# Performance work log

Measured on AMD Instinct MI355X. Metric: run time of the kernel, lower is better.

Reference implementation:

```python
import jax, jax.numpy as jnp
import numpy as np

S, IN, OUT = 2048, 512, 512
H, KV = 16, 4            # query heads, kv heads (cross-broadcast + averaged)
DQ = DK = DV = 64        # per-head embedding dims


def setup_inputs() -> dict:
    key = jax.random.key(0)
    ks = jax.random.split(key, 5)
    lim_in = 1.0 / np.sqrt(IN)
    lim_o = 1.0 / np.sqrt(H * DV)
    x = jax.random.normal(ks[0], (S, IN), dtype=jnp.float32)
    Wq = jax.random.uniform(ks[1], (H * DQ, IN), jnp.float32, -lim_in, lim_in)
    Wk = jax.random.uniform(ks[2], (KV * DK, IN), jnp.float32, -lim_in, lim_in)
    Wv = jax.random.uniform(ks[3], (KV * DV, IN), jnp.float32, -lim_in, lim_in)
    Wo = jax.random.uniform(ks[4], (OUT, H * DV), jnp.float32, -lim_o, lim_o)
    return {"x": x, "Wq": Wq, "Wk": Wk, "Wv": Wv, "Wo": Wo}


def reference(x, Wq, Wk, Wv, Wo):
    seq = x.shape[0]
    # projections (eqx.nn.Linear: y = W @ x, no bias)
    q = (x @ Wq.T).reshape(seq, H, DQ)    # [S, H, DQ]
    k = (x @ Wk.T).reshape(seq, KV, DK)   # [S, KV, DK]
    v = (x @ Wv.T).reshape(seq, KV, DV)   # [S, KV, DV]
    # cross-broadcast every kv head against every query head -> [KV, H, S, S]
    scores = jnp.einsum('shd,tkd->khst', q, k) / jnp.sqrt(jnp.asarray(DK, x.dtype))
    # NOTE: original applies causal mask whenever `mask is not None`; the
    # boolean flag is always passed, so masking is effectively always on.
    causal = jnp.tril(jnp.ones((seq, seq), dtype=bool))
    scores = jnp.where(causal, scores, -jnp.inf)
    w = jax.nn.softmax(scores, axis=-1)   # [KV, H, S, S]
    # attn @ V, then sum over kv heads and average by KV
    o = jnp.einsum('khst,tkd->shd', w, v) / KV  # [S, H, DV]
    return o.reshape(seq, H * DV) @ Wo.T        # [S, OUT]
```

## Files before the change

### kernel.cpp

```cpp
#include <hip/hip_runtime.h>
#include <hip/hip_bf16.h>

#define SEQ   2048
#define INF_  512
#define HQ    16
#define KVH   4
#define DH    64
#define NQ    (HQ*DH)
#define NKV   (KVH*DH)
#define OUTD  512

typedef short v8s __attribute__((ext_vector_type(8)));
typedef float v4f __attribute__((ext_vector_type(4)));

static __device__ __forceinline__ float bf2f(unsigned short u) {
    union { unsigned int i; float f; } c;
    c.i = ((unsigned int)u) << 16;
    return c.f;
}
static __device__ __forceinline__ unsigned short f2bf(float f) {
    union { float f; unsigned int i; } c; c.f = f;
    unsigned int lsb = (c.i >> 16) & 1u;
    c.i += 0x7fffu + lsb;
    return (unsigned short)(c.i >> 16);
}
static __device__ __forceinline__ unsigned int f2bf2(float lo, float hi) {
    union { __hip_bfloat162 h; unsigned int u; } c;
    c.h = __float22bfloat162_rn(make_float2(lo, hi));
    return c.u;
}
static __device__ __forceinline__ v8s pack8(v4f a, v4f b) {
    union { v8s s; uint4 u; } c;
    c.u = make_uint4(f2bf2(a[0], a[1]), f2bf2(a[2], a[3]),
                     f2bf2(b[0], b[1]), f2bf2(b[2], b[3]));
    return c.s;
}

static __device__ __forceinline__ void gll16(const void* g, void* l) {
    __builtin_amdgcn_global_load_lds(
        (const __attribute__((address_space(1))) void*)g,
        (__attribute__((address_space(3))) void*)l, 16, 0, 0);
}

static __device__ __forceinline__ void stage_tile(
    const unsigned short* __restrict__ src, int stride, int kb,
    unsigned short* ldsbase, int w, int lane)
{
#pragma unroll
    for (int i = 0; i < 2; i++) {
        const int rl = w * 16 + i * 8 + (lane >> 3);
        const int kc = ((lane & 7) ^ (rl & 7)) * 8;
        gll16(src + (size_t)rl * stride + kb + kc,
              ldsbase + (w * 16 + i * 8) * 64);
    }
}

static __device__ __forceinline__ void stage_tile32(
    const unsigned short* __restrict__ src, int stride, int kb,
    unsigned short* ldsbase, int w, int lane)
{
    const int rl = w * 8 + (lane >> 3);
    const int kc = ((lane & 7) ^ (rl & 7)) * 8;
    gll16(src + (size_t)rl * stride + kb + kc,
          ldsbase + (w * 8) * 64);
}

#define QSCALE 0.180336880f

__global__ __launch_bounds__(256) void cast_all(
    const float* __restrict__ x,  const float* __restrict__ Wq,
    const float* __restrict__ Wk, const float* __restrict__ Wv,
    const float* __restrict__ Wo,
    unsigned short* __restrict__ xb,  unsigned short* __restrict__ Wqb,
    unsigned short* __restrict__ Wkb, unsigned short* __restrict__ Wvb,
    unsigned short* __restrict__ Wob)
{
    size_t i = ((size_t)blockIdx.x * 256 + threadIdx.x) * 8;
    const float* s; unsigned short* d; size_t off;
    if (i < 1048576)      { s = x;  d = xb;  off = i; }
    else if (i < 1572864) { s = Wq; d = Wqb; off = i - 1048576; }
    else if (i < 1703936) { s = Wk; d = Wkb; off = i - 1572864; }
    else if (i < 1835008) { s = Wv; d = Wvb; off = i - 1703936; }
    else                  { s = Wo; d = Wob; off = i - 1835008; }
    float4 a = *(const float4*)(s + off);
    float4 b = *(const float4*)(s + off + 4);
    *(uint4*)(d + off) = make_uint4(f2bf2(a.x, a.y), f2bf2(a.z, a.w),
                                    f2bf2(b.x, b.y), f2bf2(b.z, b.w));
}

__global__ __launch_bounds__(256, 4) void gemm_qkv(
    const unsigned short* __restrict__ xb,
    const unsigned short* __restrict__ Wqb,
    const unsigned short* __restrict__ Wkb,
    const unsigned short* __restrict__ Wvb,
    unsigned short* __restrict__ Qg,
    unsigned short* __restrict__ Kg,
    unsigned short* __restrict__ Vg)
{
    __shared__ unsigned short Asb[2][4096];
    __shared__ unsigned short Bsb[2][4096];

    const int m0 = blockIdx.x * 64;
    const int n0 = blockIdx.y * 64;

    const unsigned short* Bp; int role;
    if (n0 < NQ)            { Bp = Wqb + (size_t)n0 * INF_;              role = 0; }
    else if (n0 < NQ + NKV) { Bp = Wkb + (size_t)(n0 - NQ) * INF_;       role = 1; }
    else                    { Bp = Wvb + (size_t)(n0 - NQ - NKV) * INF_; role = 2; }

    const int tid = threadIdx.x;
    const int w = tid >> 6, lane = tid & 63;
    const int n = lane & 15, quad = lane >> 4;
    const int m7 = n & 7;
    const int r0w = (w & 1) * 32, c0w = (w >> 1) * 32;
    const unsigned short* Ap = xb + (size_t)m0 * INF_;

    v4f acc[2][2];
#pragma unroll
    for (int rt = 0; rt < 2; rt++)
#pragma unroll
        for (int ct = 0; ct < 2; ct++) acc[rt][ct] = (v4f){0.f,0.f,0.f,0.f};

    stage_tile(Ap, INF_, 0, &Asb[0][0], w, lane);
    stage_tile(Bp, INF_, 0, &Bsb[0][0], w, lane);

    for (int kb = 0; kb < INF_; kb += 64) {
        const int buf = (kb >> 6) & 1;
        __syncthreads();
        if (kb + 64 < INF_) {
            stage_tile(Ap, INF_, kb + 64, &Asb[buf ^ 1][0], w, lane);
            stage_tile(Bp, INF_, kb + 64, &Bsb[buf ^ 1][0], w, lane);
        }
#pragma unroll
        for (int kk = 0; kk < 2; kk++) {
            const int gs = ((kk * 4 + quad) ^ m7) * 8;
            v8s a0 = *(const v8s*)&Asb[buf][(r0w + n) * 64 + gs];
            v8s a1 = *(const v8s*)&Asb[buf][(r0w + 16 + n) * 64 + gs];
            v8s b0 = *(const v8s*)&Bsb[buf][(c0w + n) * 64 + gs];
            v8s b1 = *(const v8s*)&Bsb[buf][(c0w + 16 + n) * 64 + gs];
            acc[0][0] = __builtin_amdgcn_mfma_f32_16x16x32_bf16(a0, b0, acc[0][0], 0, 0, 0);
            acc[0][1] = __builtin_amdgcn_mfma_f32_16x16x32_bf16(a0, b1, acc[0][1], 0, 0, 0);
            acc[1][0] = __builtin_amdgcn_mfma_f32_16x16x32_bf16(a1, b0, acc[1][0], 0, 0, 0);
            acc[1][1] = __builtin_amdgcn_mfma_f32_16x16x32_bf16(a1, b1, acc[1][1], 0, 0, 0);
        }
    }

    const int t = m0 >> 6;
    if (role == 0) {
        unsigned short* base = Qg + ((size_t)(t * 16 + (n0 >> 6))) * 4096;
#pragma unroll
        for (int rt = 0; rt < 2; rt++)
#pragma unroll
            for (int ct = 0; ct < 2; ct++)
#pragma unroll
                for (int reg = 0; reg < 4; reg++) {
                    const int r = r0w + rt * 16 + quad * 4 + reg;
                    const int d = c0w + ct * 16 + n;
                    base[r * 64 + (((d >> 3) ^ (r & 7)) * 8) + (d & 7)] =
                        f2bf(acc[rt][ct][reg] * QSCALE);
                }
    } else if (role == 1) {
        const int g = (n0 - NQ) >> 6;
        unsigned short* base = Kg + ((size_t)(g * 32 + t)) * 4096;
#pragma unroll
        for (int rt = 0; rt < 2; rt++)
#pragma unroll
            for (int ct = 0; ct < 2; ct++)
#pragma unroll
                for (int reg = 0; reg < 4; reg++) {
                    const int r = r0w + rt * 16 + quad * 4 + reg;
                    const int d = c0w + ct * 16 + n;
                    base[r * 64 + (((d >> 3) ^ (r & 7)) * 8) + (d & 7)] =
                        f2bf(acc[rt][ct][reg]);
                }
    } else {
        const int g = (n0 - NQ - NKV) >> 6;
        unsigned short* base = Vg + ((size_t)(g * 32 + t)) * 4096;
#pragma unroll
        for (int rt = 0; rt < 2; rt++)
#pragma unroll
            for (int ct = 0; ct < 2; ct++) {
                const int jb_ = r0w + rt * 16 + quad * 4;
                const int d = c0w + ct * 16 + n;
                const int p = (jb_ & 32) + (((jb_ >> 2) & 3) * 8) + (((jb_ >> 4) & 1) * 4);
                *(uint2*)&base[d * 64 + (((p >> 3) ^ (d & 7)) * 8) + (p & 7)] =
                    make_uint2(f2bf2(acc[rt][ct][0], acc[rt][ct][1]),
                               f2bf2(acc[rt][ct][2], acc[rt][ct][3]));
            }
    }
}

__global__ __launch_bounds__(256, 4) void attn_mfma(
    const unsigned short* __restrict__ Qg,
    const unsigned short* __restrict__ Kg,
    const unsigned short* __restrict__ Vg,
    unsigned short* __restrict__ Oh)
{
    __shared__ unsigned short Ksb[2][4096];
    __shared__ unsigned short Vsb[2][4096];

    const int bx = blockIdx.x;
    const int h  = bx & 15;
    const int p  = (bx >> 4) & 7;
    const int sp = (bx >> 7) & 1;
    const int g  = bx >> 8;
    const int tid = threadIdx.x;
    const int w = tid >> 6, lane = tid & 63;
    const int n = lane & 15, quad = lane >> 4;
    const int m7 = n & 7;

    v8s ones;
#pragma unroll
    for (int i = 0; i < 8; i++) ones[i] = (short)0x3F80;
    const v4f z = (v4f){0.f,0.f,0.f,0.f};

    unsigned short* Ohp = Oh + (size_t)g * ((size_t)SEQ * NQ);

    for (int half = 0; half < 2; half++) {
        const int qi2 = half ? (15 - p) : p;
        const int qbase = qi2 * 128 + sp * 64;
        const int ext = 2 * qi2 + sp + 1;
        const int rowbase = qbase + w * 16;

        if (half) __syncthreads();

        {
            const size_t off = ((size_t)(g * 32)) * 4096 + w * 1024 + lane * 8;
            gll16(Kg + off,       &Ksb[0][w * 1024]);
            gll16(Kg + off + 512, &Ksb[0][w * 1024 + 512]);
            gll16(Vg + off,       &Vsb[0][w * 1024]);
            gll16(Vg + off + 512, &Vsb[0][w * 1024 + 512]);
        }

        v8s qf0, qf1;
        {
            const unsigned short* rp =
                Qg + ((size_t)((2 * qi2 + sp) * 16 + h)) * 4096 + (w * 16 + n) * 64;
            qf0 = *(const v8s*)(rp + (quad ^ m7) * 8);
            qf1 = *(const v8s*)(rp + ((quad + 4) ^ m7) * 8);
        }

        v4f Lacc = (v4f){0.f,0.f,0.f,0.f};
        v4f Oacc[4];
#pragma unroll
        for (int dt = 0; dt < 4; dt++) Oacc[dt] = (v4f){0.f,0.f,0.f,0.f};

        for (int tt = 0; tt < ext; tt++) {
            const int buf = tt & 1;
            __syncthreads();
            if (tt + 1 < ext) {
                const size_t off = ((size_t)(g * 32 + tt + 1)) * 4096 + w * 1024 + lane * 8;
                const int nb = buf ^ 1;
                gll16(Kg + off,       &Ksb[nb][w * 1024]);
                gll16(Kg + off + 512, &Ksb[nb][w * 1024 + 512]);
                gll16(Vg + off,       &Vsb[nb][w * 1024]);
                gll16(Vg + off + 512, &Vsb[nb][w * 1024 + 512]);
            }
            const int t0 = tt * 64;
            const unsigned short* Kb = Ksb[buf];
            const unsigned short* Vb = Vsb[buf];

            v4f sc[4];
            __builtin_amdgcn_s_setprio(1);
#pragma unroll
            for (int jt = 0; jt < 4; jt++) {
                const int kr = (jt * 16 + n) * 64;
                v8s kf0 = *(const v8s*)&Kb[kr + (quad ^ m7) * 8];
                v8s kf1 = *(const v8s*)&Kb[kr + ((quad + 4) ^ m7) * 8];
                v4f tq = __builtin_amdgcn_mfma_f32_16x16x32_bf16(kf0, qf0, z, 0, 0, 0);
                sc[jt] = __builtin_amdgcn_mfma_f32_16x16x32_bf16(kf1, qf1, tq, 0, 0, 0);
            }
            __builtin_amdgcn_s_setprio(0);

            if (t0 + 63 > rowbase) {
                const int qg = rowbase + n;
#pragma unroll
                for (int jt = 0; jt < 4; jt++) {
                    const int jg = t0 + jt * 16 + quad * 4;
#pragma unroll
                    for (int reg = 0; reg < 4; reg++)
                        sc[jt][reg] = (jg + reg <= qg) ? sc[jt][reg] : -INFINITY;
                }
            }
#pragma unroll
            for (int jt = 0; jt < 4; jt++)
#pragma unroll
                for (int reg = 0; reg < 4; reg++)
                    sc[jt][reg] = __builtin_amdgcn_exp2f(sc[jt][reg]);

            v8s pf0 = pack8(sc[0], sc[1]);
            v8s pf1 = pack8(sc[2], sc[3]);

            __builtin_amdgcn_s_setprio(1);
            Lacc = __builtin_amdgcn_mfma_f32_16x16x32_bf16(ones, pf0, Lacc, 0, 0, 0);
            Lacc = __builtin_amdgcn_mfma_f32_16x16x32_bf16(ones, pf1, Lacc, 0, 0, 0);

#pragma unroll
            for (int dt = 0; dt < 4; dt++) {
                const int vr = (dt * 16 + n) * 64;
                v8s vf0 = *(const v8s*)&Vb[vr + (quad ^ m7) * 8];
                v8s vf1 = *(const v8s*)&Vb[vr + ((quad + 4) ^ m7) * 8];
                Oacc[dt] = __builtin_amdgcn_mfma_f32_16x16x32_bf16(vf0, pf0, Oacc[dt], 0, 0, 0);
                Oacc[dt] = __builtin_amdgcn_mfma_f32_16x16x32_bf16(vf1, pf1, Oacc[dt], 0, 0, 0);
            }
            __builtin_amdgcn_s_setprio(0);
        }

        {
            const float inv = 0.25f / Lacc[0];
            const int row = rowbase + n;
            unsigned short* dst = Ohp + (size_t)row * NQ + h * DH + quad * 4;
#pragma unroll
            for (int dt = 0; dt < 4; dt++) {
                uint2 pk = make_uint2(f2bf2(Oacc[dt][0] * inv, Oacc[dt][1] * inv),
                                      f2bf2(Oacc[dt][2] * inv, Oacc[dt][3] * inv));
                *(uint2*)(dst + dt * 16) = pk;
            }
        }
    }
}

__global__ __launch_bounds__(256) void sum4(
    const unsigned short* __restrict__ Oh,
    unsigned short* __restrict__ Os)
{
    const size_t i = ((size_t)blockIdx.x * 256 + threadIdx.x) * 8;
    const size_t plane = (size_t)SEQ * NQ;
    uint4 u0 = *(const uint4*)(Oh + i);
    uint4 u1 = *(const uint4*)(Oh + plane + i);
    uint4 u2 = *(const uint4*)(Oh + 2 * plane + i);
    uint4 u3 = *(const uint4*)(Oh + 3 * plane + i);
    unsigned int ow[4];
#pragma unroll
    for (int q = 0; q < 4; q++) {
        const unsigned int a = ((const unsigned int*)&u0)[q];
        const unsigned int b = ((const unsigned int*)&u1)[q];
        const unsigned int c = ((const unsigned int*)&u2)[q];
        const unsigned int d = ((const unsigned int*)&u3)[q];
        float lo = bf2f((unsigned short)(a & 0xffffu)) + bf2f((unsigned short)(b & 0xffffu))
                 + bf2f((unsigned short)(c & 0xffffu)) + bf2f((unsigned short)(d & 0xffffu));
        float hi = bf2f((unsigned short)(a >> 16)) + bf2f((unsigned short)(b >> 16))
                 + bf2f((unsigned short)(c >> 16)) + bf2f((unsigned short)(d >> 16));
        ow[q] = f2bf2(lo, hi);
    }
    *(uint4*)(Os + i) = make_uint4(ow[0], ow[1], ow[2], ow[3]);
}

__global__ __launch_bounds__(256, 4) void gemm_out(
    const unsigned short* __restrict__ Os,
    const unsigned short* __restrict__ Wob,
    float* __restrict__ C)
{
    __shared__ unsigned short Asb[2][2048];
    __shared__ unsigned short Bsb[2][4096];

    const int m0 = blockIdx.x * 32;
    const int n0 = blockIdx.y * 64;
    const int tid = threadIdx.x;
    const int w = tid >> 6, lane = tid & 63;
    const int n = lane & 15, quad = lane >> 4;
    const int m7 = n & 7;
    const int rw = (w & 1) * 16, cw = (w >> 1) * 32;

    const unsigned short* Ap = Os + (size_t)m0 * NQ;
    const unsigned short* Bp = Wob + (size_t)n0 * NQ;

    v4f acc[2];
    acc[0] = (v4f){0.f,0.f,0.f,0.f};
    acc[1] = (v4f){0.f,0.f,0.f,0.f};

    stage_tile32(Ap, NQ, 0, &Asb[0][0], w, lane);
    stage_tile  (Bp, NQ, 0, &Bsb[0][0], w, lane);

    for (int kb = 0; kb < NQ; kb += 64) {
        const int buf = (kb >> 6) & 1;
        __syncthreads();
        if (kb + 64 < NQ) {
            stage_tile32(Ap, NQ, kb + 64, &Asb[buf ^ 1][0], w, lane);
            stage_tile  (Bp, NQ, kb + 64, &Bsb[buf ^ 1][0], w, lane);
        }
#pragma unroll
        for (int kk = 0; kk < 2; kk++) {
            const int gs = ((kk * 4 + quad) ^ m7) * 8;
            v8s a  = *(const v8s*)&Asb[buf][(rw + n) * 64 + gs];
            v8s b0 = *(const v8s*)&Bsb[buf][(cw + n) * 64 + gs];
            v8s b1 = *(const v8s*)&Bsb[buf][(cw + 16 + n) * 64 + gs];
            acc[0] = __builtin_amdgcn_mfma_f32_16x16x32_bf16(a, b0, acc[0], 0, 0, 0);
            acc[1] = __builtin_amdgcn_mfma_f32_16x16x32_bf16(a, b1, acc[1], 0, 0, 0);
        }
    }

#pragma unroll
    for (int ct = 0; ct < 2; ct++)
#pragma unroll
        for (int reg = 0; reg < 4; reg++) {
            const int row = m0 + rw + quad * 4 + reg;
            const int col = n0 + cw + ct * 16 + n;
            C[(size_t)row * OUTD + col] = acc[ct][reg];
        }
}

extern "C" void kernel_launch(void* const* d_in, const int* in_sizes, int n_in,
                              void* d_out, int out_size, void* d_ws, size_t ws_size,
                              hipStream_t stream) {
    const float* x  = (const float*)d_in[0];
    const float* Wq = (const float*)d_in[1];
    const float* Wk = (const float*)d_in[2];
    const float* Wv = (const float*)d_in[3];
    const float* Wo = (const float*)d_in[4];
    float* out = (float*)d_out;

    char* base = (char*)d_ws;
    unsigned short* Oh  = (unsigned short*)(base);
    unsigned short* xb  = (unsigned short*)(base);
    unsigned short* Wqb = (unsigned short*)(base + 2097152);
    unsigned short* Wkb = (unsigned short*)(base + 3145728);
    unsigned short* Wvb = (unsigned short*)(base + 3407872);
    unsigned short* Qg  = (unsigned short*)(base + 16777216);
    unsigned short* Kg  = (unsigned short*)(base + 20971520);
    unsigned short* Vg  = (unsigned short*)(base + 22020096);
    unsigned short* Wob = (unsigned short*)(base + 23068672);
    unsigned short* Os  = Qg;

    dim3 blk(256);
    cast_all<<<dim3(1152), blk, 0, stream>>>(x, Wq, Wk, Wv, Wo,
                                             xb, Wqb, Wkb, Wvb, Wob);
    gemm_qkv<<<dim3(SEQ / 64, (NQ + 2 * NKV) / 64), blk, 0, stream>>>(
        xb, Wqb, Wkb, Wvb, Qg, Kg, Vg);
    attn_mfma<<<dim3(1024), blk, 0, stream>>>(Qg, Kg, Vg, Oh);
    sum4<<<dim3(1024), blk, 0, stream>>>(Oh, Os);
    gemm_out<<<dim3(SEQ / 32, OUTD / 64), blk, 0, stream>>>(Os, Wob, out);
}
```

Baseline: 142.7 us.

## Software-pipeline QK^T scores one tile ahead of softmax and PV

Restructures the attention inner loop so the QK^T MFMAs for tile t are issued in the same iteration as the mask/exp2/PV work for tile t-1. V gets a third LDS buffer so its tile stays live one extra iteration, and the global base pointers are hoisted. The aim is to overlap the exp/pack latency with matrix work. In exchange it adds LDS (one more 8 KB buffer), more live registers, and an extra loop iteration, which may lower occupancy under launch_bounds(256,4). It also leaves a dead modulo computation in the prefetch index.

```diff
diff --git a/kernel.cpp b/kernel.cpp
--- a/kernel.cpp
+++ b/kernel.cpp
@@ -197,7 +197,7 @@
     unsigned short* __restrict__ Oh)
 {
     __shared__ unsigned short Ksb[2][4096];
-    __shared__ unsigned short Vsb[2][4096];
+    __shared__ unsigned short Vsb[3][4096];
 
     const int bx = blockIdx.x;
     const int h  = bx & 15;
@@ -215,6 +215,8 @@
     const v4f z = (v4f){0.f,0.f,0.f,0.f};
 
     unsigned short* Ohp = Oh + (size_t)g * ((size_t)SEQ * NQ);
+    const unsigned short* Kgp = Kg + ((size_t)(g * 32)) * 4096 + w * 1024 + lane * 8;
+    const unsigned short* Vgp = Vg + ((size_t)(g * 32)) * 4096 + w * 1024 + lane * 8;
 
     for (int half = 0; half < 2; half++) {
         const int qi2 = half ? (15 - p) : p;
@@ -224,13 +226,10 @@
 
         if (half) __syncthreads();
 
-        {
-            const size_t off = ((size_t)(g * 32)) * 4096 + w * 1024 + lane * 8;
-            gll16(Kg + off,       &Ksb[0][w * 1024]);
-            gll16(Kg + off + 512, &Ksb[0][w * 1024 + 512]);
-            gll16(Vg + off,       &Vsb[0][w * 1024]);
-            gll16(Vg + off + 512, &Vsb[0][w * 1024 + 512]);
-        }
+        gll16(Kgp,       &Ksb[0][w * 1024]);
+        gll16(Kgp + 512, &Ksb[0][w * 1024 + 512]);
+        gll16(Vgp,       &Vsb[0][w * 1024]);
+        gll16(Vgp + 512, &Vsb[0][w * 1024 + 512]);
 
         v8s qf0, qf1;
         {
@@ -245,65 +244,99 @@
 #pragma unroll
         for (int dt = 0; dt < 4; dt++) Oacc[dt] = (v4f){0.f,0.f,0.f,0.f};
 
-        for (int tt = 0; tt < ext; tt++) {
-            const int buf = tt & 1;
+        v4f scP0, scP1, scP2, scP3;
+        scP0 = scP1 = scP2 = scP3 = z;
+
+        for (int t = 0; t <= ext; t++) {
+            const int kbuf = t & 1;
             __syncthreads();
-            if (tt + 1 < ext) {
-                const size_t off = ((size_t)(g * 32 + tt + 1)) * 4096 + w * 1024 + lane * 8;
-                const int nb = buf ^ 1;
-                gll16(Kg + off,       &Ksb[nb][w * 1024]);
-                gll16(Kg + off + 512, &Ksb[nb][w * 1024 + 512]);
-                gll16(Vg + off,       &Vsb[nb][w * 1024]);
-                gll16(Vg + off + 512, &Vsb[nb][w * 1024 + 512]);
+            if (t + 1 < ext) {
+                const int kb2 = (t + 1) & 1;
+                int vb2 = t + 1; vb2 -= (vb2 >= 3) ? 3 : 0; vb2 -= (vb2 >= 3) ? 3 : 0;
+                vb2 = (t + 1) % 3;
+                const size_t doff = (size_t)(t + 1) * 4096;
+                gll16(Kgp + doff,       &Ksb[kb2][w * 1024]);
+                gll16(Kgp + doff + 512, &Ksb[kb2][w * 1024 + 512]);
+                gll16(Vgp + doff,       &Vsb[vb2][w * 1024]);
+                gll16(Vgp + doff + 512, &Vsb[vb2][w * 1024 + 512]);
             }
-            const int t0 = tt * 64;
-            const unsigned short* Kb = Ksb[buf];
-            const unsigned short* Vb = Vsb[buf];
-
-            v4f sc[4];
-            __builtin_amdgcn_s_setprio(1);
-#pragma unroll
-            for (int jt = 0; jt < 4; jt++) {
-                const int kr = (jt * 16 + n) * 64;
-                v8s kf0 = *(const v8s*)&Kb[kr + (quad ^ m7) * 8];
-                v8s kf1 = *(const v8s*)&Kb[kr + ((quad + 4) ^ m7) * 8];
-                v4f tq = __builtin_amdgcn_mfma_f32_16x16x32_bf16(kf0, qf0, z, 0, 0, 0);
-                sc[jt] = __builtin_amdgcn_mfma_f32_16x16x32_bf16(kf1, qf1, tq, 0, 0, 0);
+
+            v4f scN0 = z, scN1 = z, scN2 = z, scN3 = z;
+            if (t < ext) {
+                const unsigned short* Kb = Ksb[kbuf];
+                __builtin_amdgcn_s_setprio(1);
+                {
+                    const int kr0 = n * 64;
+                    v8s ka = *(const v8s*)&Kb[kr0 + (quad ^ m7) * 8];
+                    v8s kb_ = *(const v8s*)&Kb[kr0 + ((quad + 4) ^ m7) * 8];
+                    v4f tq = __builtin_amdgcn_mfma_f32_16x16x32_bf16(ka, qf0, z, 0, 0, 0);
+                    scN0 = __builtin_amdgcn_mfma_f32_16x16x32_bf16(kb_, qf1, tq, 0, 0, 0);
+                }
+                {
+                    const int kr1 = (16 + n) * 64;
+                    v8s ka = *(const v8s*)&Kb[kr1 + (quad ^ m7) * 8];
+                    v8s kb_ = *(const v8s*)&Kb[kr1 + ((quad + 4) ^ m7) * 8];
+                    v4f tq = __builtin_amdgcn_mfma_f32_16x16x32_bf16(ka, qf0, z, 0, 0, 0);
+                    scN1 = __builtin_amdgcn_mfma_f32_16x16x32_bf16(kb_, qf1, tq, 0, 0, 0);
+                }
+                {
+                    const int kr2 = (32 + n) * 64;
+                    v8s ka = *(const v8s*)&Kb[kr2 + (quad ^ m7) * 8];
+                    v8s kb_ = *(const v8s*)&Kb[kr2 + ((quad + 4) ^ m7) * 8];
+                    v4f tq = __builtin_amdgcn_mfma_f32_16x16x32_bf16(ka, qf0, z, 0, 0, 0);
+                    scN2 = __builtin_amdgcn_mfma_f32_16x16x32_bf16(kb_, qf1, tq, 0, 0, 0);
+                }
+                {
+                    const int kr3 = (48 + n) * 64;
+                    v8s ka = *(const v8s*)&Kb[kr3 + (quad ^ m7) * 8];
+                    v8s kb_ = *(const v8s*)&Kb[kr3 + ((quad + 4) ^ m7) * 8];
+                    v4f tq = __builtin_amdgcn_mfma_f32_16x16x32_bf16(ka, qf0, z, 0, 0, 0);
+                    scN3 = __builtin_amdgcn_mfma_f32_16x16x32_bf16(kb_, qf1, tq, 0, 0, 0);
+                }
+                __builtin_amdgcn_s_setprio(0);
             }
-            __builtin_amdgcn_s_setprio(0);
-
-            if (t0 + 63 > rowbase) {
-                const int qg = rowbase + n;
-#pragma unroll
-                for (int jt = 0; jt < 4; jt++) {
-                    const int jg = t0 + jt * 16 + quad * 4;
-#pragma unroll
-                    for (int reg = 0; reg < 4; reg++)
-                        sc[jt][reg] = (jg + reg <= qg) ? sc[jt][reg] : -INFINITY;
-                }
+
+            if (t > 0) {
+                const int tp = t - 1;
+                const int t0 = tp * 64;
+                v4f s0 = scP0, s1 = scP1, s2 = scP2, s3 = scP3;
+                if (t0 + 63 > rowbase) {
+                    const int qg = rowbase + n;
+#pragma unroll
+                    for (int reg = 0; reg < 4; reg++) {
+                        s0[reg] = (t0 +  0 + quad * 4 + reg <= qg) ? s0[reg] : -INFINITY;
+                        s1[reg] = (t0 + 16 + quad * 4 + reg <= qg) ? s1[reg] : -INFINITY;
+                        s2[reg] = (t0 + 32 + quad * 4 + reg <= qg) ? s2[reg] : -INFINITY;
+                        s3[reg] = (t0 + 48 + quad * 4 + reg <= qg) ? s3[reg] : -INFINITY;
+                    }
+                }
+#pragma unroll
+                for (int reg = 0; reg < 4; reg++) {
+                    s0[reg] = __builtin_amdgcn_exp2f(s0[reg]);
+                    s1[reg] = __builtin_amdgcn_exp2f(s1[reg]);
+                    s2[reg] = __builtin_amdgcn_exp2f(s2[reg]);
+                    s3[reg] = __builtin_amdgcn_exp2f(s3[reg]);
+                }
+                v8s pf0 = pack8(s0, s1);
+                v8s pf1 = pack8(s2, s3);
+
+                __builtin_amdgcn_s_setprio(1);
+                Lacc = __builtin_amdgcn_mfma_f32_16x16x32_bf16(ones, pf0, Lacc, 0, 0, 0);
+                Lacc = __builtin_amdgcn_mfma_f32_16x16x32_bf16(ones, pf1, Lacc, 0, 0, 0);
+
+                const unsigned short* Vb = Vsb[tp % 3];
+#pragma unroll
+                for (int dt = 0; dt < 4; dt++) {
+                    const int vr = (dt * 16 + n) * 64;
+                    v8s vf0 = *(const v8s*)&Vb[vr + (quad ^ m7) * 8];
+                    v8s vf1 = *(const v8s*)&Vb[vr + ((quad + 4) ^ m7) * 8];
+                    Oacc[dt] = __builtin_amdgcn_mfma_f32_16x16x32_bf16(vf0, pf0, Oacc[dt], 0, 0, 0);
+                    Oacc[dt] = __builtin_amdgcn_mfma_f32_16x16x32_bf16(vf1, pf1, Oacc[dt], 0, 0, 0);
+                }
+                __builtin_amdgcn_s_setprio(0);
             }
-#pragma unroll
-            for (int jt = 0; jt < 4; jt++)
-#pragma unroll
-                for (int reg = 0; reg < 4; reg++)
-                    sc[jt][reg] = __builtin_amdgcn_exp2f(sc[jt][reg]);
-
-            v8s pf0 = pack8(sc[0], sc[1]);
-            v8s pf1 = pack8(sc[2], sc[3]);
-
-            __builtin_amdgcn_s_setprio(1);
-            Lacc = __builtin_amdgcn_mfma_f32_16x16x32_bf16(ones, pf0, Lacc, 0, 0, 0);
-            Lacc = __builtin_amdgcn_mfma_f32_16x16x32_bf16(ones, pf1, Lacc, 0, 0, 0);
-
-#pragma unroll
-            for (int dt = 0; dt < 4; dt++) {
-                const int vr = (dt * 16 + n) * 64;
-                v8s vf0 = *(const v8s*)&Vb[vr + (quad ^ m7) * 8];
-                v8s vf1 = *(const v8s*)&Vb[vr + ((quad + 4) ^ m7) * 8];
-                Oacc[dt] = __builtin_amdgcn_mfma_f32_16x16x32_bf16(vf0, pf0, Oacc[dt], 0, 0, 0);
-                Oacc[dt] = __builtin_amdgcn_mfma_f32_16x16x32_bf16(vf1, pf1, Oacc[dt], 0, 0, 0);
-            }
-            __builtin_amdgcn_s_setprio(0);
+
+            scP0 = scN0; scP1 = scN1; scP2 = scN2; scP3 = scN3;
         }
 
         {
```

Result: no change. 145.1 us (+1.7%).

## Load K/V fragments directly from global memory instead of LDS staging

Applied to the files above, without the earlier changes.

Removes the double-buffered shared-memory staging of K and V tiles and their per-tile barriers. Each wave now reads its K and V MFMA fragments straight from global memory (relying on L1/L2 caching), with the loop body manually unrolled. This eliminates LDS traffic and __syncthreads, but each of the four waves now issues redundant global loads for the same tile, and load latency is no longer hidden by a prefetch.

```diff
diff --git a/kernel.cpp b/kernel.cpp
--- a/kernel.cpp
+++ b/kernel.cpp
@@ -196,9 +196,6 @@
     const unsigned short* __restrict__ Vg,
     unsigned short* __restrict__ Oh)
 {
-    __shared__ unsigned short Ksb[2][4096];
-    __shared__ unsigned short Vsb[2][4096];
-
     const int bx = blockIdx.x;
     const int h  = bx & 15;
     const int p  = (bx >> 4) & 7;
@@ -208,6 +205,8 @@
     const int w = tid >> 6, lane = tid & 63;
     const int n = lane & 15, quad = lane >> 4;
     const int m7 = n & 7;
+    const int fo0 = (quad ^ m7) * 8;
+    const int fo1 = ((quad + 4) ^ m7) * 8;
 
     v8s ones;
 #pragma unroll
@@ -215,29 +214,20 @@
     const v4f z = (v4f){0.f,0.f,0.f,0.f};
 
     unsigned short* Ohp = Oh + (size_t)g * ((size_t)SEQ * NQ);
+    const unsigned short* Kg0 = Kg + (size_t)(g * 32) * 4096;
+    const unsigned short* Vg0 = Vg + (size_t)(g * 32) * 4096;
 
     for (int half = 0; half < 2; half++) {
         const int qi2 = half ? (15 - p) : p;
-        const int qbase = qi2 * 128 + sp * 64;
         const int ext = 2 * qi2 + sp + 1;
-        const int rowbase = qbase + w * 16;
-
-        if (half) __syncthreads();
-
-        {
-            const size_t off = ((size_t)(g * 32)) * 4096 + w * 1024 + lane * 8;
-            gll16(Kg + off,       &Ksb[0][w * 1024]);
-            gll16(Kg + off + 512, &Ksb[0][w * 1024 + 512]);
-            gll16(Vg + off,       &Vsb[0][w * 1024]);
-            gll16(Vg + off + 512, &Vsb[0][w * 1024 + 512]);
-        }
+        const int rowbase = qi2 * 128 + sp * 64 + w * 16;
 
         v8s qf0, qf1;
         {
             const unsigned short* rp =
                 Qg + ((size_t)((2 * qi2 + sp) * 16 + h)) * 4096 + (w * 16 + n) * 64;
-            qf0 = *(const v8s*)(rp + (quad ^ m7) * 8);
-            qf1 = *(const v8s*)(rp + ((quad + 4) ^ m7) * 8);
+            qf0 = *(const v8s*)(rp + fo0);
+            qf1 = *(const v8s*)(rp + fo1);
         }
 
         v4f Lacc = (v4f){0.f,0.f,0.f,0.f};
@@ -245,64 +235,82 @@
 #pragma unroll
         for (int dt = 0; dt < 4; dt++) Oacc[dt] = (v4f){0.f,0.f,0.f,0.f};
 
-        for (int tt = 0; tt < ext; tt++) {
-            const int buf = tt & 1;
-            __syncthreads();
-            if (tt + 1 < ext) {
-                const size_t off = ((size_t)(g * 32 + tt + 1)) * 4096 + w * 1024 + lane * 8;
-                const int nb = buf ^ 1;
-                gll16(Kg + off,       &Ksb[nb][w * 1024]);
-                gll16(Kg + off + 512, &Ksb[nb][w * 1024 + 512]);
-                gll16(Vg + off,       &Vsb[nb][w * 1024]);
-                gll16(Vg + off + 512, &Vsb[nb][w * 1024 + 512]);
-            }
-            const int t0 = tt * 64;
-            const unsigned short* Kb = Ksb[buf];
-            const unsigned short* Vb = Vsb[buf];
-
-            v4f sc[4];
+        for (int t = 0; t < ext; t++) {
+            const unsigned short* Kt = Kg0 + (size_t)t * 4096;
+            const unsigned short* Vt = Vg0 + (size_t)t * 4096;
+
+            v8s kf00 = *(const v8s*)&Kt[( 0 + n) * 64 + fo0];
+            v8s kf01 = *(const v8s*)&Kt[( 0 + n) * 64 + fo1];
+            v8s kf10 = *(const v8s*)&Kt[(16 + n) * 64 + fo0];
+            v8s kf11 = *(const v8s*)&Kt[(16 + n) * 64 + fo1];
+            v8s kf20 = *(const v8s*)&Kt[(32 + n) * 64 + fo0];
+            v8s kf21 = *(const v8s*)&Kt[(32 + n) * 64 + fo1];
+            v8s kf30 = *(const v8s*)&Kt[(48 + n) * 64 + fo0];
+            v8s kf31 = *(const v8s*)&Kt[(48 + n) * 64 + fo1];
+
+            v4f sc0, sc1, sc2, sc3;
             __builtin_amdgcn_s_setprio(1);
-#pragma unroll
-            for (int jt = 0; jt < 4; jt++) {
-                const int kr = (jt * 16 + n) * 64;
-                v8s kf0 = *(const v8s*)&Kb[kr + (quad ^ m7) * 8];
-                v8s kf1 = *(const v8s*)&Kb[kr + ((quad + 4) ^ m7) * 8];
-                v4f tq = __builtin_amdgcn_mfma_f32_16x16x32_bf16(kf0, qf0, z, 0, 0, 0);
-                sc[jt] = __builtin_amdgcn_mfma_f32_16x16x32_bf16(kf1, qf1, tq, 0, 0, 0);
+            {
+                v4f tq = __builtin_amdgcn_mfma_f32_16x16x32_bf16(kf00, qf0, z, 0, 0, 0);
+                sc0 = __builtin_amdgcn_mfma_f32_16x16x32_bf16(kf01, qf1, tq, 0, 0, 0);
+            }
+            {
+                v4f tq = __builtin_amdgcn_mfma_f32_16x16x32_bf16(kf10, qf0, z, 0, 0, 0);
+                sc1 = __builtin_amdgcn_mfma_f32_16x16x32_bf16(kf11, qf1, tq, 0, 0, 0);
+            }
+            {
+                v4f tq = __builtin_amdgcn_mfma_f32_16x16x32_bf16(kf20, qf0, z, 0, 0, 0);
+                sc2 = __builtin_amdgcn_mfma_f32_16x16x32_bf16(kf21, qf1, tq, 0, 0, 0);
+            }
+            {
+                v4f tq = __builtin_amdgcn_mfma_f32_16x16x32_bf16(kf30, qf0, z, 0, 0, 0);
+                sc3 = __builtin_amdgcn_mfma_f32_16x16x32_bf16(kf31, qf1, tq, 0, 0, 0);
             }
             __builtin_amdgcn_s_setprio(0);
 
+            v8s vf00 = *(const v8s*)&Vt[( 0 + n) * 64 + fo0];
+            v8s vf01 = *(const v8s*)&Vt[( 0 + n) * 64 + fo1];
+            v8s vf10 = *(const v8s*)&Vt[(16 + n) * 64 + fo0];
+            v8s vf11 = *(const v8s*)&Vt[(16 + n) * 64 + fo1];
+            v8s vf20 = *(const v8s*)&Vt[(32 + n) * 64 + fo0];
+            v8s vf21 = *(const v8s*)&Vt[(32 + n) * 64 + fo1];
+            v8s vf30 = *(const v8s*)&Vt[(48 + n) * 64 + fo0];
+            v8s vf31 = *(const v8s*)&Vt[(48 + n) * 64 + fo1];
+
+            const int t0 = t * 64;
             if (t0 + 63 > rowbase) {
                 const int qg = rowbase + n;
 #pragma unroll
-                for (int jt = 0; jt < 4; jt++) {
-                    const int jg = t0 + jt * 16 + quad * 4;
-#pragma unroll
-                    for (int reg = 0; reg < 4; reg++)
-                        sc[jt][reg] = (jg + reg <= qg) ? sc[jt][reg] : -INFINITY;
+                for (int reg = 0; reg < 4; reg++) {
+                    sc0[reg] = (t0 +  0 + quad * 4 + reg <= qg) ? sc0[reg] : -INFINITY;
+                    sc1[reg] = (t0 + 16 + quad * 4 + reg <= qg) ? sc1[reg] : -INFINITY;
+                    sc2[reg] = (t0 + 32 + quad * 4 + reg <= qg) ? sc2[reg] : -INFINITY;
+                    sc3[reg] = (t0 + 48 + quad * 4 + reg <= qg) ? sc3[reg] : -INFINITY;
                 }
             }
 #pragma unroll
-            for (int jt = 0; jt < 4; jt++)
-#pragma unroll
-                for (int reg = 0; reg < 4; reg++)
-                    sc[jt][reg] = __builtin_amdgcn_exp2f(sc[jt][reg]);
-
-            v8s pf0 = pack8(sc[0], sc[1]);
-            v8s pf1 = pack8(sc[2], sc[3]);
+            for (int reg = 0; reg < 4; reg++) {
+                sc0[reg] = __builtin_amdgcn_exp2f(sc0[reg]);
+                sc1[reg] = __builtin_amdgcn_exp2f(sc1[reg]);
+                sc2[reg] = __builtin_amdgcn_exp2f(sc2[reg]);
+                sc3[reg] = __builtin_amdgcn_exp2f(sc3[reg]);
+            }
+
+            v8s pf0 = pack8(sc0, sc1);
+            v8s pf1 = pack8(sc2, sc3);
 
             __builtin_amdgcn_s_setprio(1);
             Lacc = __builtin_amdgcn_mfma_f32_16x16x32_bf16(ones, pf0, Lacc, 0, 0, 0);
             Lacc = __builtin_amdgcn_mfma_f32_16x16x32_bf16(ones, pf1, Lacc, 0, 0, 0);
 
-#pragma unroll
-            for (int dt = 0; dt < 4; dt++) {
-                const int vr = (dt * 16 + n) * 64;
-                v8s vf0 = *(const v8s*)&Vb[vr + (quad ^ m7) * 8];
-                v8s vf1 = *(const v8s*)&Vb[vr + ((quad + 4) ^ m7) * 8];
-                Oacc[dt] = __builtin_amdgcn_mfma_f32_16x16x32_bf16(vf0, pf0, Oacc[dt], 0, 0, 0);
-                Oacc[dt] = __builtin_amdgcn_mfma_f32_16x16x32_bf16(vf1, pf1, Oacc[dt], 0, 0, 0);
-            }
+            Oacc[0] = __builtin_amdgcn_mfma_f32_16x16x32_bf16(vf00, pf0, Oacc[0], 0, 0, 0);
+            Oacc[0] = __builtin_amdgcn_mfma_f32_16x16x32_bf16(vf01, pf1, Oacc[0], 0, 0, 0);
+            Oacc[1] = __builtin_amdgcn_mfma_f32_16x16x32_bf16(vf10, pf0, Oacc[1], 0, 0, 0);
+            Oacc[1] = __builtin_amdgcn_mfma_f32_16x16x32_bf16(vf11, pf1, Oacc[1], 0, 0, 0);
+            Oacc[2] = __builtin_amdgcn_mfma_f32_16x16x32_bf16(vf20, pf0, Oacc[2], 0, 0, 0);
+            Oacc[2] = __builtin_amdgcn_mfma_f32_16x16x32_bf16(vf21, pf1, Oacc[2], 0, 0, 0);
+            Oacc[3] = __builtin_amdgcn_mfma_f32_16x16x32_bf16(vf30, pf0, Oacc[3], 0, 0, 0);
+            Oacc[3] = __builtin_amdgcn_mfma_f32_16x16x32_bf16(vf31, pf1, Oacc[3], 0, 0, 0);
             __builtin_amdgcn_s_setprio(0);
         }
 
```

After: 194.7 us. 1.36x slower.

## Process two query heads per attention block to reuse K/V tiles

Applied to the files above, without the earlier changes.

Each attention block now handles a pair of query heads against the same KV head, so every K/V tile staged in shared memory and every K/V fragment read from LDS feeds twice as many MFMAs. The grid is halved and the launch bound relaxed to two blocks per SM to make room for the doubled accumulators and Q fragments. This aims to cut global and LDS traffic per unit of compute, at the cost of fewer blocks, higher register pressure and lower occupancy.

```diff
diff --git a/kernel.cpp b/kernel.cpp
--- a/kernel.cpp
+++ b/kernel.cpp
@@ -190,7 +190,7 @@
     }
 }
 
-__global__ __launch_bounds__(256, 4) void attn_mfma(
+__global__ __launch_bounds__(256, 2) void attn_mfma(
     const unsigned short* __restrict__ Qg,
     const unsigned short* __restrict__ Kg,
     const unsigned short* __restrict__ Vg,
@@ -200,14 +200,16 @@
     __shared__ unsigned short Vsb[2][4096];
 
     const int bx = blockIdx.x;
-    const int h  = bx & 15;
-    const int p  = (bx >> 4) & 7;
-    const int sp = (bx >> 7) & 1;
-    const int g  = bx >> 8;
+    const int hg = bx & 7;
+    const int p  = (bx >> 3) & 7;
+    const int sp = (bx >> 6) & 1;
+    const int g  = bx >> 7;
     const int tid = threadIdx.x;
     const int w = tid >> 6, lane = tid & 63;
     const int n = lane & 15, quad = lane >> 4;
     const int m7 = n & 7;
+    const int fo0 = (quad ^ m7) * 8;
+    const int fo1 = ((quad + 4) ^ m7) * 8;
 
     v8s ones;
 #pragma unroll
@@ -218,9 +220,8 @@
 
     for (int half = 0; half < 2; half++) {
         const int qi2 = half ? (15 - p) : p;
-        const int qbase = qi2 * 128 + sp * 64;
         const int ext = 2 * qi2 + sp + 1;
-        const int rowbase = qbase + w * 16;
+        const int rowbase = qi2 * 128 + sp * 64 + w * 16;
 
         if (half) __syncthreads();
 
@@ -232,18 +233,22 @@
             gll16(Vg + off + 512, &Vsb[0][w * 1024 + 512]);
         }
 
-        v8s qf0, qf1;
+        v8s qa0, qa1, qb0, qb1;
         {
-            const unsigned short* rp =
-                Qg + ((size_t)((2 * qi2 + sp) * 16 + h)) * 4096 + (w * 16 + n) * 64;
-            qf0 = *(const v8s*)(rp + (quad ^ m7) * 8);
-            qf1 = *(const v8s*)(rp + ((quad + 4) ^ m7) * 8);
-        }
-
-        v4f Lacc = (v4f){0.f,0.f,0.f,0.f};
-        v4f Oacc[4];
-#pragma unroll
-        for (int dt = 0; dt < 4; dt++) Oacc[dt] = (v4f){0.f,0.f,0.f,0.f};
+            const unsigned short* rpA =
+                Qg + ((size_t)((2 * qi2 + sp) * 16 + hg * 2)) * 4096 + (w * 16 + n) * 64;
+            const unsigned short* rpB = rpA + 4096;
+            qa0 = *(const v8s*)(rpA + fo0);
+            qa1 = *(const v8s*)(rpA + fo1);
+            qb0 = *(const v8s*)(rpB + fo0);
+            qb1 = *(const v8s*)(rpB + fo1);
+        }
+
+        v4f LA = (v4f){0.f,0.f,0.f,0.f};
+        v4f LB = (v4f){0.f,0.f,0.f,0.f};
+        v4f OA[4], OB[4];
+#pragma unroll
+        for (int dt = 0; dt < 4; dt++) { OA[dt] = z; OB[dt] = z; }
 
         for (int tt = 0; tt < ext; tt++) {
             const int buf = tt & 1;
@@ -256,65 +261,83 @@
                 gll16(Vg + off,       &Vsb[nb][w * 1024]);
                 gll16(Vg + off + 512, &Vsb[nb][w * 1024 + 512]);
             }
-            const int t0 = tt * 64;
             const unsigned short* Kb = Ksb[buf];
             const unsigned short* Vb = Vsb[buf];
 
-            v4f sc[4];
+            v4f sa[4], sb[4];
             __builtin_amdgcn_s_setprio(1);
 #pragma unroll
             for (int jt = 0; jt < 4; jt++) {
                 const int kr = (jt * 16 + n) * 64;
-                v8s kf0 = *(const v8s*)&Kb[kr + (quad ^ m7) * 8];
-                v8s kf1 = *(const v8s*)&Kb[kr + ((quad + 4) ^ m7) * 8];
-                v4f tq = __builtin_amdgcn_mfma_f32_16x16x32_bf16(kf0, qf0, z, 0, 0, 0);
-                sc[jt] = __builtin_amdgcn_mfma_f32_16x16x32_bf16(kf1, qf1, tq, 0, 0, 0);
+                v8s k0 = *(const v8s*)&Kb[kr + fo0];
+                v8s k1 = *(const v8s*)&Kb[kr + fo1];
+                v4f ta = __builtin_amdgcn_mfma_f32_16x16x32_bf16(k0, qa0, z, 0, 0, 0);
+                sa[jt] = __builtin_amdgcn_mfma_f32_16x16x32_bf16(k1, qa1, ta, 0, 0, 0);
+                v4f tb = __builtin_amdgcn_mfma_f32_16x16x32_bf16(k0, qb0, z, 0, 0, 0);
+                sb[jt] = __builtin_amdgcn_mfma_f32_16x16x32_bf16(k1, qb1, tb, 0, 0, 0);
             }
             __builtin_amdgcn_s_setprio(0);
 
+            const int t0 = tt * 64;
             if (t0 + 63 > rowbase) {
                 const int qg = rowbase + n;
 #pragma unroll
                 for (int jt = 0; jt < 4; jt++) {
                     const int jg = t0 + jt * 16 + quad * 4;
 #pragma unroll
-                    for (int reg = 0; reg < 4; reg++)
-                        sc[jt][reg] = (jg + reg <= qg) ? sc[jt][reg] : -INFINITY;
+                    for (int reg = 0; reg < 4; reg++) {
+                        const bool keep = (jg + reg <= qg);
+                        sa[jt][reg] = keep ? sa[jt][reg] : -INFINITY;
+                        sb[jt][reg] = keep ? sb[jt][reg] : -INFINITY;
+                    }
                 }
             }
 #pragma unroll
             for (int jt = 0; jt < 4; jt++)
 #pragma unroll
-                for (int reg = 0; reg < 4; reg++)
-                    sc[jt][reg] = __builtin_amdgcn_exp2f(sc[jt][reg]);
-
-            v8s pf0 = pack8(sc[0], sc[1]);
-            v8s pf1 = pack8(sc[2], sc[3]);
+                for (int reg = 0; reg < 4; reg++) {
+                    sa[jt][reg] = __builtin_amdgcn_exp2f(sa[jt][reg]);
+                    sb[jt][reg] = __builtin_amdgcn_exp2f(sb[jt][reg]);
+                }
+
+            v8s pA0 = pack8(sa[0], sa[1]);
+            v8s pA1 = pack8(sa[2], sa[3]);
+            v8s pB0 = pack8(sb[0], sb[1]);
+            v8s pB1 = pack8(sb[2], sb[3]);
 
             __builtin_amdgcn_s_setprio(1);
-            Lacc = __builtin_amdgcn_mfma_f32_16x16x32_bf16(ones, pf0, Lacc, 0, 0, 0);
-            Lacc = __builtin_amdgcn_mfma_f32_16x16x32_bf16(ones, pf1, Lacc, 0, 0, 0);
+            LA = __builtin_amdgcn_mfma_f32_16x16x32_bf16(ones, pA0, LA, 0, 0, 0);
+            LA = __builtin_amdgcn_mfma_f32_16x16x32_bf16(ones, pA1, LA, 0, 0, 0);
+            LB = __builtin_amdgcn_mfma_f32_16x16x32_bf16(ones, pB0, LB, 0, 0, 0);
+            LB = __builtin_amdgcn_mfma_f32_16x16x32_bf16(ones, pB1, LB, 0, 0, 0);
 
 #pragma unroll
             for (int dt = 0; dt < 4; dt++) {
                 const int vr = (dt * 16 + n) * 64;
-                v8s vf0 = *(const v8s*)&Vb[vr + (quad ^ m7) * 8];
-                v8s vf1 = *(const v8s*)&Vb[vr + ((quad + 4) ^ m7) * 8];
-                Oacc[dt] = __builtin_amdgcn_mfma_f32_16x16x32_bf16(vf0, pf0, Oacc[dt], 0, 0, 0);
-                Oacc[dt] = __builtin_amdgcn_mfma_f32_16x16x32_bf16(vf1, pf1, Oacc[dt], 0, 0, 0);
+                v8s v0 = *(const v8s*)&Vb[vr + fo0];
+                v8s v1 = *(const v8s*)&Vb[vr + fo1];
+                OA[dt] = __builtin_amdgcn_mfma_f32_16x16x32_bf16(v0, pA0, OA[dt], 0, 0, 0);
+                OA[dt] = __builtin_amdgcn_mfma_f32_16x16x32_bf16(v1, pA1, OA[dt], 0, 0, 0);
+                OB[dt] = __builtin_amdgcn_mfma_f32_16x16x32_bf16(v0, pB0, OB[dt], 0, 0, 0);
+                OB[dt] = __builtin_amdgcn_mfma_f32_16x16x32_bf16(v1, pB1, OB[dt], 0, 0, 0);
             }
             __builtin_amdgcn_s_setprio(0);
         }
 
         {
-            const float inv = 0.25f / Lacc[0];
+            const float invA = 0.25f / LA[0];
+            const float invB = 0.25f / LB[0];
             const int row = rowbase + n;
-            unsigned short* dst = Ohp + (size_t)row * NQ + h * DH + quad * 4;
+            unsigned short* dA = Ohp + (size_t)row * NQ + (hg * 2) * DH + quad * 4;
+            unsigned short* dB = dA + DH;
 #pragma unroll
             for (int dt = 0; dt < 4; dt++) {
-                uint2 pk = make_uint2(f2bf2(Oacc[dt][0] * inv, Oacc[dt][1] * inv),
-                                      f2bf2(Oacc[dt][2] * inv, Oacc[dt][3] * inv));
-                *(uint2*)(dst + dt * 16) = pk;
+                uint2 pkA = make_uint2(f2bf2(OA[dt][0] * invA, OA[dt][1] * invA),
+                                       f2bf2(OA[dt][2] * invA, OA[dt][3] * invA));
+                *(uint2*)(dA + dt * 16) = pkA;
+                uint2 pkB = make_uint2(f2bf2(OB[dt][0] * invB, OB[dt][1] * invB),
+                                       f2bf2(OB[dt][2] * invB, OB[dt][3] * invB));
+                *(uint2*)(dB + dt * 16) = pkB;
             }
         }
     }
@@ -427,7 +450,7 @@
                                              xb, Wqb, Wkb, Wvb, Wob);
     gemm_qkv<<<dim3(SEQ / 64, (NQ + 2 * NKV) / 64), blk, 0, stream>>>(
         xb, Wqb, Wkb, Wvb, Qg, Kg, Vg);
-    attn_mfma<<<dim3(1024), blk, 0, stream>>>(Qg, Kg, Vg, Oh);
+    attn_mfma<<<dim3(512), blk, 0, stream>>>(Qg, Kg, Vg, Oh);
     sum4<<<dim3(1024), blk, 0, stream>>>(Oh, Os);
     gemm_out<<<dim3(SEQ / 32, OUTD / 64), blk, 0, stream>>>(Os, Wob, out);
 }
```

Measured after the change: 139.3 us. 2.4% less time.
